# Kernel tuning notes

Measured on AMD Instinct MI355X. Metric: run time of the kernel, lower is better.

Reference implementation:

```python
import jax, jax.numpy as jnp
import numpy as np

B, T, P = 16, 200, 100          # batch, timesteps, MAX_CODE_LEN paths
EMB = 100                        # per-table embedding dim
D = 3 * EMB                      # concatenated path-context dim = 300
NODE_VOCAB = 20000 + 2
PATH_VOCAB = 50000 + 2
SKILL = 30                       # self.skill_n
Q = 50                           # questions (rnn_first_part width)
OUT = 50                         # output_dim


def setup_inputs() -> dict:
    key = jax.random.key(0)
    ks = jax.random.split(key, 14)
    lin = lambda k, fi, fo: jax.random.uniform(k, (fi, fo), jnp.float32, -1.0, 1.0) / np.sqrt(fi)
    vec = lambda k, fi, fo: jax.random.uniform(k, (fo,), jnp.float32, -1.0, 1.0) / np.sqrt(fi)
    return {
        "x_float": jax.random.normal(ks[0], (B, T, Q), jnp.float32),
        "c2v_idx": jax.random.randint(ks[1], (B, T, P, 3), 0, NODE_VOCAB, jnp.int32),
        "embed_nodes": jax.random.normal(ks[2], (NODE_VOCAB, EMB), jnp.float32),
        "embed_paths": jax.random.normal(ks[3], (PATH_VOCAB, EMB), jnp.float32),
        "W_trans": lin(ks[4], D, D), "b_trans": vec(ks[5], D, D),
        "W_att": lin(ks[6], D, 1), "b_att": vec(ks[7], D, 1),
        "W_skill": lin(ks[8], D, SKILL), "b_skill": vec(ks[9], D, SKILL),
        "W_kc": lin(ks[10], Q, SKILL) + 0.15, "b_kc": vec(ks[11], Q, SKILL),
        "W_pred": lin(ks[12], SKILL, OUT), "b_pred": vec(ks[13], SKILL, OUT),
    }


def reference(x_float, c2v_idx, embed_nodes, embed_paths, W_trans, b_trans,
              W_att, b_att, W_skill, b_skill, W_kc, b_kc, W_pred, b_pred):
    # gather three embeddings per path triple  -> [B,T,P,100] each
    start_e = embed_nodes[c2v_idx[..., 0]]
    path_e = embed_paths[c2v_idx[..., 1]]
    end_e = embed_nodes[c2v_idx[..., 2]]
    full_embed = jnp.concatenate([start_e, end_e, path_e], axis=-1)   # [B,T,P,300]

    # path transformation + attention scores
    transformed = jnp.tanh(full_embed @ W_trans + b_trans)            # [B,T,P,300]
    context_w = transformed @ W_att + b_att                           # [B,T,P,1]
    # NOTE: original uses nn.Softmax(dim=1) -> softmax over the TIME axis
    attn = jax.nn.softmax(context_w, axis=1)                          # [B,T,P,1]
    code_vectors = jnp.sum(full_embed * attn, axis=2)                 # [B,T,300]

    kc_mask = jax.nn.sigmoid(x_float @ W_kc + b_kc)                   # [B,T,30]
    out = code_vectors @ W_skill + b_skill                            # [B,T,30]
    res2 = out * (kc_mask >= 0.5).astype(out.dtype)                   # hard-gated skills
    res = jax.nn.sigmoid(res2 @ W_pred + b_pred)                      # [B,T,50]
    return (res, res2, kc_mask, attn)
```

## Files before the change

### kernel.cpp

```cpp
#include <hip/hip_runtime.h>
#include <hip/hip_bf16.h>
#include <math.h>

#define Bdim 16
#define Tdim 200
#define Pdim 100
#define EMB  100
#define Ddim 300
#define SKILL 30
#define Qdim 50
#define OUTD 50

#define OFF_RES   0
#define OFF_RES2  (Bdim*Tdim*OUTD)
#define OFF_KC    (OFF_RES2 + Bdim*Tdim*SKILL)
#define OFF_ATTN  (OFF_KC + Bdim*Tdim*SKILL)

typedef __bf16 bf16x8 __attribute__((ext_vector_type(8)));
typedef __bf16 bf16x4 __attribute__((ext_vector_type(4)));
typedef float  f32x4  __attribute__((ext_vector_type(4)));

#define BM    128
#define KPAD  320
#define ASTR  312
#define TPB   512

#define EROW  320

#define NROWS (Bdim*Tdim*Pdim)
#define WBT_BYTES ((size_t)KPAD*KPAD*2)
#define E_BYTES   ((size_t)NROWS*EROW*2)

__device__ __forceinline__ float fast_tanh(float x) {
    float t = __expf(2.0f * x);
    return 1.0f - 2.0f * __builtin_amdgcn_rcpf(t + 1.0f);
}
__device__ __forceinline__ float sigmoidf_(float z) {
    return 1.f / (1.f + expf(-z));
}

__global__ __launch_bounds__(256) void prep_wbt_kernel(
    const float* __restrict__ Wt, __bf16* __restrict__ wbt)
{
    int id = blockIdx.x * 256 + threadIdx.x;
    if (id >= KPAD * KPAD) return;
    int j = id / KPAD, k = id - j * KPAD;
    float v = (j < Ddim && k < Ddim) ? Wt[k * Ddim + j] : 0.0f;
    wbt[id] = (__bf16)v;
}

template <bool WRITE_E>
__global__ __launch_bounds__(TPB, 4) void score_mfma_kernel(
    const int*    __restrict__ c2v,
    const float*  __restrict__ en,
    const float*  __restrict__ ep,
    const __bf16* __restrict__ wbt,
    const float*  __restrict__ bt,
    const float*  __restrict__ wa,
    const float*  __restrict__ ba,
    float* __restrict__ scores,
    __bf16* __restrict__ e_out)
{
    __shared__ __align__(16) __bf16 A_lds[BM * ASTR];
    __shared__ __align__(16) char   aux_lds[2048];
    int*  idx_lds = (int*)aux_lds;
    float (*red_lds)[BM] = (float (*)[BM])aux_lds;

    const int tid = threadIdx.x;
    const int m0  = blockIdx.x * BM;

    if (tid < BM * 3) idx_lds[tid] = c2v[(size_t)m0 * 3 + tid];
    __syncthreads();

    {
        const int r   = tid >> 2;
        const int sub = tid & 3;
        const int i0 = idx_lds[r * 3 + 0];
        const int i1 = idx_lds[r * 3 + 1];
        const int i2 = idx_lds[r * 3 + 2];
        __bf16* arow = &A_lds[r * ASTR];
        const float* srcs[3] = { en + (size_t)i0 * EMB,
                                 en + (size_t)i2 * EMB,
                                 ep + (size_t)i1 * EMB };
        #pragma unroll
        for (int seg = 0; seg < 3; ++seg) {
            const float* src = srcs[seg];
            float4 v[7];
            #pragma unroll
            for (int k = 0; k < 7; ++k) {
                int j = sub + 4 * k;
                if (j < 25) v[k] = *(const float4*)(src + j * 4);
            }
            #pragma unroll
            for (int k = 0; k < 7; ++k) {
                int j = sub + 4 * k;
                if (j < 25) {
                    float4 w = v[k];
                    bf16x4 b4 = { (__bf16)w.x, (__bf16)w.y, (__bf16)w.z, (__bf16)w.w };
                    *(bf16x4*)(arow + seg * 100 + j * 4) = b4;
                }
            }
        }
        if (sub < 3) *(bf16x4*)(arow + 300 + sub * 4) = (bf16x4){};
    }
    __syncthreads();

    if (WRITE_E) {
        #pragma unroll
        for (int pos = tid; pos < BM * 40; pos += TPB) {
            int r = pos / 40, q = pos - r * 40;
            bf16x8 v = *(const bf16x8*)&A_lds[r * ASTR + q * 8];
            *(bf16x8*)&e_out[(size_t)(m0 + r) * EROW + q * 8] = v;
        }
    }

    const int wid = tid >> 6, lane = tid & 63;
    const int wm = wid >> 2, wn = wid & 3;
    const int lr = lane & 15, lg = lane >> 4;

    f32x4 acc[4][5];
    #pragma unroll
    for (int mf = 0; mf < 4; ++mf)
        #pragma unroll
        for (int nf = 0; nf < 5; ++nf) acc[mf][nf] = (f32x4){0.f, 0.f, 0.f, 0.f};

    #pragma unroll
    for (int kt = 0; kt < 10; ++kt) {
        const int k0 = kt * 32;
        bf16x8 bfr[5];
        #pragma unroll
        for (int nf = 0; nf < 5; ++nf)
            bfr[nf] = *(const bf16x8*)&wbt[(size_t)(wn * 80 + nf * 16 + lr) * KPAD + k0 + lg * 8];
        bf16x8 af[4];
        #pragma unroll
        for (int mf = 0; mf < 4; ++mf) {
            bf16x8 a = *(const bf16x8*)&A_lds[(wm * 64 + mf * 16 + lr) * ASTR + k0 + lg * 8];
            if (kt == 9 && lg == 3) a = (bf16x8){};
            af[mf] = a;
        }
        #pragma unroll
        for (int mf = 0; mf < 4; ++mf)
            #pragma unroll
            for (int nf = 0; nf < 5; ++nf)
                acc[mf][nf] = __builtin_amdgcn_mfma_f32_16x16x32_bf16(
                    af[mf], bfr[nf], acc[mf][nf], 0, 0, 0);
    }

    float btv[5], wav[5];
    #pragma unroll
    for (int nf = 0; nf < 5; ++nf) {
        int c = wn * 80 + nf * 16 + lr;
        bool ok = (c < Ddim);
        btv[nf] = ok ? bt[c] : 0.f;
        wav[nf] = ok ? wa[c] : 0.f;
    }
    float sred[4][4];
    #pragma unroll
    for (int mf = 0; mf < 4; ++mf) {
        #pragma unroll
        for (int i = 0; i < 4; ++i) {
            float s = 0.f;
            #pragma unroll
            for (int nf = 0; nf < 5; ++nf)
                s += fast_tanh(acc[mf][nf][i] + btv[nf]) * wav[nf];
            s += __shfl_xor(s, 1, 64);
            s += __shfl_xor(s, 2, 64);
            s += __shfl_xor(s, 4, 64);
            s += __shfl_xor(s, 8, 64);
            sred[mf][i] = s;
        }
    }
    __syncthreads();
    #pragma unroll
    for (int mf = 0; mf < 4; ++mf)
        #pragma unroll
        for (int i = 0; i < 4; ++i)
            if (lr == 0) red_lds[wn][wm * 64 + mf * 16 + lg * 4 + i] = sred[mf][i];
    __syncthreads();
    for (int r = tid; r < BM; r += TPB) {
        float s = ba[0] + red_lds[0][r] + red_lds[1][r] + red_lds[2][r] + red_lds[3][r];
        scores[m0 + r] = s;
    }
}

__global__ __launch_bounds__(64) void softmax_time_kernel(float* __restrict__ a)
{
    const int b = blockIdx.x / Pdim;
    const int p = blockIdx.x - b * Pdim;
    const int lane = threadIdx.x;
    const size_t base = (size_t)b * Tdim * Pdim + p;

    float v[4];
    float m = -1e30f;
    #pragma unroll
    for (int i = 0; i < 4; ++i) {
        int t = lane + i * 64;
        v[i] = (t < Tdim) ? a[base + (size_t)t * Pdim] : -1e30f;
        m = fmaxf(m, v[i]);
    }
    #pragma unroll
    for (int off = 32; off > 0; off >>= 1) m = fmaxf(m, __shfl_xor(m, off, 64));

    float s = 0.f;
    #pragma unroll
    for (int i = 0; i < 4; ++i) {
        int t = lane + i * 64;
        if (t < Tdim) { v[i] = expf(v[i] - m); s += v[i]; }
    }
    #pragma unroll
    for (int off = 32; off > 0; off >>= 1) s += __shfl_xor(s, off, 64);

    const float inv = 1.f / s;
    #pragma unroll
    for (int i = 0; i < 4; ++i) {
        int t = lane + i * 64;
        if (t < Tdim) a[base + (size_t)t * Pdim] = v[i] * inv;
    }
}

template <bool USE_E>
__global__ __launch_bounds__(512, 4) void cvpred4_kernel(
    const float*  __restrict__ x,
    const int*    __restrict__ c2v,
    const float*  __restrict__ en,
    const float*  __restrict__ ep,
    const __bf16* __restrict__ E,
    const float*  __restrict__ attn,
    const float* __restrict__ Wsk, const float* __restrict__ bsk,
    const float* __restrict__ Wkc, const float* __restrict__ bkc,
    const float* __restrict__ Wpr, const float* __restrict__ bpr,
    float* __restrict__ res, float* __restrict__ res2, float* __restrict__ kcm)
{
    const int bt_i = blockIdx.x;
    const int tid  = threadIdx.x;

    __shared__ float  wsk_lds[Ddim * SKILL];
    __shared__ float  wkc_lds[Qdim * SKILL];
    __shared__ float  wpr_lds[SKILL * OUTD];
    __shared__ int    idx_lds[Pdim * 3];
    __shared__ float  attn_lds[Pdim];
    __shared__ float  x_lds[Qdim];
    __shared__ float4 part_lds[6][76];
    __shared__ float  cv_lds[Ddim];
    __shared__ float  zk_lds[SKILL], o_lds[SKILL], r2_lds[SKILL];

    const int pg = tid / 75;
    const int ch = tid - pg * 75;

    for (int i = tid; i < (Ddim * SKILL) / 4; i += 512)
        ((float4*)wsk_lds)[i] = ((const float4*)Wsk)[i];
    for (int i = tid; i < (Qdim * SKILL) / 4; i += 512)
        ((float4*)wkc_lds)[i] = ((const float4*)Wkc)[i];
    for (int i = tid; i < (SKILL * OUTD) / 4; i += 512)
        ((float4*)wpr_lds)[i] = ((const float4*)Wpr)[i];
    if (!USE_E) {
        if (tid < Pdim * 3) idx_lds[tid] = c2v[(size_t)bt_i * (Pdim * 3) + tid];
    }
    if (tid >= 320 && tid < 320 + Pdim) attn_lds[tid - 320] = attn[(size_t)bt_i * Pdim + tid - 320];
    if (tid >= 448 && tid < 448 + Qdim) x_lds[tid - 448] = x[(size_t)bt_i * Qdim + tid - 448];

    bf16x4 ev[17];
    if (USE_E && pg < 6) {
        const __bf16* base = E + (size_t)bt_i * (Pdim * EROW) + ch * 4;
        #pragma unroll
        for (int k = 0; k < 17; ++k) {
            int p = pg + 6 * k;
            if (p < Pdim) ev[k] = *(const bf16x4*)(base + p * EROW);
        }
    }
    __syncthreads();

    if (pg < 6) {
        float4 acc = {0.f, 0.f, 0.f, 0.f};
        if (USE_E) {
            #pragma unroll
            for (int k = 0; k < 17; ++k) {
                int p = pg + 6 * k;
                if (p < Pdim) {
                    float a = attn_lds[p];
                    acc.x = fmaf(a, (float)ev[k].x, acc.x);
                    acc.y = fmaf(a, (float)ev[k].y, acc.y);
                    acc.z = fmaf(a, (float)ev[k].z, acc.z);
                    acc.w = fmaf(a, (float)ev[k].w, acc.w);
                }
            }
        } else {
            const int seg = ch / 25, cq = ch - seg * 25;
            const float* tab = (seg == 2) ? ep : en;
            const int io = (seg == 0) ? 0 : (seg == 1) ? 2 : 1;
            int   ri[17];
            float rw[17];
            #pragma unroll
            for (int k = 0; k < 17; ++k) {
                int p = pg + 6 * k;
                bool ok = (p < Pdim);
                ri[k] = idx_lds[(ok ? p : 0) * 3 + io];
                rw[k] = ok ? attn_lds[p] : 0.f;
            }
            {
                float4 va[9];
                #pragma unroll
                for (int k = 0; k < 9; ++k)
                    va[k] = *(const float4*)&tab[(size_t)ri[k] * EMB + cq * 4];
                #pragma unroll
                for (int k = 0; k < 9; ++k) {
                    acc.x = fmaf(rw[k], va[k].x, acc.x);
                    acc.y = fmaf(rw[k], va[k].y, acc.y);
                    acc.z = fmaf(rw[k], va[k].z, acc.z);
                    acc.w = fmaf(rw[k], va[k].w, acc.w);
                }
            }
            {
                float4 vb[8];
                #pragma unroll
                for (int k = 0; k < 8; ++k)
                    vb[k] = *(const float4*)&tab[(size_t)ri[k + 9] * EMB + cq * 4];
                #pragma unroll
                for (int k = 0; k < 8; ++k) {
                    acc.x = fmaf(rw[k + 9], vb[k].x, acc.x);
                    acc.y = fmaf(rw[k + 9], vb[k].y, acc.y);
                    acc.z = fmaf(rw[k + 9], vb[k].z, acc.z);
                    acc.w = fmaf(rw[k + 9], vb[k].w, acc.w);
                }
            }
        }
        part_lds[pg][ch] = acc;
    }
    __syncthreads();

    if (tid < 75) {
        float4 a0 = part_lds[0][tid], a1 = part_lds[1][tid];
        float4 a2 = part_lds[2][tid], a3 = part_lds[3][tid];
        float4 a4 = part_lds[4][tid], a5 = part_lds[5][tid];
        int c = tid * 4;
        cv_lds[c + 0] = a0.x + a1.x + a2.x + a3.x + a4.x + a5.x;
        cv_lds[c + 1] = a0.y + a1.y + a2.y + a3.y + a4.y + a5.y;
        cv_lds[c + 2] = a0.z + a1.z + a2.z + a3.z + a4.z + a5.z;
        cv_lds[c + 3] = a0.w + a1.w + a2.w + a3.w + a4.w + a5.w;
    }
    __syncthreads();

    if (tid < 480) {
        const int s = tid >> 4, l = tid & 15;
        float o = 0.f;
        #pragma unroll
        for (int j = 0; j < 19; ++j) {
            int c = l + 16 * j;
            if (c < Ddim) o = fmaf(cv_lds[c], wsk_lds[c * SKILL + s], o);
        }
        o += __shfl_xor(o, 8, 64);
        o += __shfl_xor(o, 4, 64);
        o += __shfl_xor(o, 2, 64);
        o += __shfl_xor(o, 1, 64);
        if (l == 0) o_lds[s] = o + bsk[s];
    }
    if (tid < 240) {
        const int s = tid >> 3, l = tid & 7;
        float zk = 0.f;
        #pragma unroll
        for (int j = 0; j < 7; ++j) {
            int q = l + 8 * j;
            if (q < Qdim) zk = fmaf(x_lds[q], wkc_lds[q * SKILL + s], zk);
        }
        zk += __shfl_xor(zk, 4, 64);
        zk += __shfl_xor(zk, 2, 64);
        zk += __shfl_xor(zk, 1, 64);
        if (l == 0) zk_lds[s] = zk + bkc[s];
    }
    __syncthreads();

    if (tid < SKILL) {
        float zk = zk_lds[tid];
        float r2 = (zk >= 0.f) ? o_lds[tid] : 0.f;
        kcm [(size_t)bt_i * SKILL + tid] = sigmoidf_(zk);
        res2[(size_t)bt_i * SKILL + tid] = r2;
        r2_lds[tid] = r2;
    }
    __syncthreads();

    if (tid < 400) {
        const int od = tid >> 3, l = tid & 7;
        float z = 0.f;
        #pragma unroll
        for (int j = 0; j < 4; ++j) {
            int s = l + 8 * j;
            if (s < SKILL) z = fmaf(r2_lds[s], wpr_lds[s * OUTD + od], z);
        }
        z += __shfl_xor(z, 4, 64);
        z += __shfl_xor(z, 2, 64);
        z += __shfl_xor(z, 1, 64);
        if (l == 0) res[(size_t)bt_i * OUTD + od] = sigmoidf_(z + bpr[od]);
    }
}

extern "C" void kernel_launch(void* const* d_in, const int* in_sizes, int n_in,
                              void* d_out, int out_size, void* d_ws, size_t ws_size,
                              hipStream_t stream)
{
    const float* x   = (const float*)d_in[0];
    const int*   c2v = (const int*)  d_in[1];
    const float* en  = (const float*)d_in[2];
    const float* ep  = (const float*)d_in[3];
    const float* Wt  = (const float*)d_in[4];
    const float* bt  = (const float*)d_in[5];
    const float* Wa  = (const float*)d_in[6];
    const float* ba  = (const float*)d_in[7];
    const float* Wsk = (const float*)d_in[8];
    const float* bsk = (const float*)d_in[9];
    const float* Wkc = (const float*)d_in[10];
    const float* bkc = (const float*)d_in[11];
    const float* Wpr = (const float*)d_in[12];
    const float* bpr = (const float*)d_in[13];

    float* out  = (float*)d_out;
    float* res  = out + OFF_RES;
    float* res2 = out + OFF_RES2;
    float* kcm  = out + OFF_KC;
    float* attn = out + OFF_ATTN;

    __bf16* wbt  = (__bf16*)d_ws;
    __bf16* e_ws = (__bf16*)((char*)d_ws + WBT_BYTES);

    const bool use_e = ws_size >= WBT_BYTES + E_BYTES;

    prep_wbt_kernel<<<(KPAD * KPAD + 255) / 256, 256, 0, stream>>>(Wt, wbt);

    if (use_e)
        score_mfma_kernel<true><<<NROWS / BM, TPB, 0, stream>>>(
            c2v, en, ep, wbt, bt, Wa, ba, attn, e_ws);
    else
        score_mfma_kernel<false><<<NROWS / BM, TPB, 0, stream>>>(
            c2v, en, ep, wbt, bt, Wa, ba, attn, e_ws);

    softmax_time_kernel<<<Bdim * Pdim, 64, 0, stream>>>(attn);

    if (use_e)
        cvpred4_kernel<true><<<Bdim * Tdim, 512, 0, stream>>>(
            x, c2v, en, ep, e_ws, attn, Wsk, bsk, Wkc, bkc, Wpr, bpr, res, res2, kcm);
    else
        cvpred4_kernel<false><<<Bdim * Tdim, 512, 0, stream>>>(
            x, c2v, en, ep, e_ws, attn, Wsk, bsk, Wkc, bkc, Wpr, bpr, res, res2, kcm);
}
```

Before: 328.0 us.

## Precompute per-path skill projections in score GEMM instead of storing embeddings

Uses linearity: the attention-weighted sum of embeddings projected by W_skill equals the attention-weighted sum of per-path projections. W_skill is appended to the bf16 weight matrix, and the score MFMA kernel computes a 32-wide per-path skill projection that it writes to workspace, replacing the 320-wide bf16 embedding dump. A new cvpred5 kernel then only reduces 30 values per path instead of 300, which cuts workspace write and read traffic. The cost is extra MFMAs in two of the four N-wave groups and bf16 rounding applied before the skill projection.

```diff
diff --git a/kernel.cpp b/kernel.cpp
--- a/kernel.cpp
+++ b/kernel.cpp
@@ -22,14 +22,15 @@
 
 #define BM    128
 #define KPAD  320
+#define WROWS 352
 #define ASTR  312
 #define TPB   512
 
-#define EROW  320
+#define ESW   32
 
 #define NROWS (Bdim*Tdim*Pdim)
-#define WBT_BYTES ((size_t)KPAD*KPAD*2)
-#define E_BYTES   ((size_t)NROWS*EROW*2)
+#define WBT_BYTES ((size_t)WROWS*KPAD*2)
+#define ES_BYTES  ((size_t)NROWS*ESW*4)
 
 __device__ __forceinline__ float fast_tanh(float x) {
     float t = __expf(2.0f * x);
@@ -40,16 +41,23 @@
 }
 
 __global__ __launch_bounds__(256) void prep_wbt_kernel(
-    const float* __restrict__ Wt, __bf16* __restrict__ wbt)
+    const float* __restrict__ Wt, const float* __restrict__ Wsk,
+    __bf16* __restrict__ wbt)
 {
     int id = blockIdx.x * 256 + threadIdx.x;
-    if (id >= KPAD * KPAD) return;
+    if (id >= WROWS * KPAD) return;
     int j = id / KPAD, k = id - j * KPAD;
-    float v = (j < Ddim && k < Ddim) ? Wt[k * Ddim + j] : 0.0f;
+    float v = 0.0f;
+    if (j < KPAD) {
+        if (j < Ddim && k < Ddim) v = Wt[k * Ddim + j];
+    } else {
+        int s = j - KPAD;
+        if (s < SKILL && k < Ddim) v = Wsk[k * SKILL + s];
+    }
     wbt[id] = (__bf16)v;
 }
 
-template <bool WRITE_E>
+template <bool WRITE_ES>
 __global__ __launch_bounds__(TPB, 4) void score_mfma_kernel(
     const int*    __restrict__ c2v,
     const float*  __restrict__ en,
@@ -59,7 +67,7 @@
     const float*  __restrict__ wa,
     const float*  __restrict__ ba,
     float* __restrict__ scores,
-    __bf16* __restrict__ e_out)
+    float* __restrict__ es_out)
 {
     __shared__ __align__(16) __bf16 A_lds[BM * ASTR];
     __shared__ __align__(16) char   aux_lds[2048];
@@ -105,24 +113,19 @@
     }
     __syncthreads();
 
-    if (WRITE_E) {
-        #pragma unroll
-        for (int pos = tid; pos < BM * 40; pos += TPB) {
-            int r = pos / 40, q = pos - r * 40;
-            bf16x8 v = *(const bf16x8*)&A_lds[r * ASTR + q * 8];
-            *(bf16x8*)&e_out[(size_t)(m0 + r) * EROW + q * 8] = v;
-        }
-    }
-
     const int wid = tid >> 6, lane = tid & 63;
     const int wm = wid >> 2, wn = wid & 3;
     const int lr = lane & 15, lg = lane >> 4;
+    const bool do_es = WRITE_ES && (wn < 2);
 
     f32x4 acc[4][5];
-    #pragma unroll
-    for (int mf = 0; mf < 4; ++mf)
+    f32x4 acc_es[4];
+    #pragma unroll
+    for (int mf = 0; mf < 4; ++mf) {
         #pragma unroll
         for (int nf = 0; nf < 5; ++nf) acc[mf][nf] = (f32x4){0.f, 0.f, 0.f, 0.f};
+        acc_es[mf] = (f32x4){0.f, 0.f, 0.f, 0.f};
+    }
 
     #pragma unroll
     for (int kt = 0; kt < 10; ++kt) {
@@ -144,6 +147,24 @@
             for (int nf = 0; nf < 5; ++nf)
                 acc[mf][nf] = __builtin_amdgcn_mfma_f32_16x16x32_bf16(
                     af[mf], bfr[nf], acc[mf][nf], 0, 0, 0);
+        if (do_es) {
+            bf16x8 bes = *(const bf16x8*)&wbt[(size_t)(KPAD + wn * 16 + lr) * KPAD + k0 + lg * 8];
+            #pragma unroll
+            for (int mf = 0; mf < 4; ++mf)
+                acc_es[mf] = __builtin_amdgcn_mfma_f32_16x16x32_bf16(
+                    af[mf], bes, acc_es[mf], 0, 0, 0);
+        }
+    }
+
+    if (do_es) {
+        #pragma unroll
+        for (int mf = 0; mf < 4; ++mf)
+            #pragma unroll
+            for (int i = 0; i < 4; ++i) {
+                int row = wm * 64 + mf * 16 + lg * 4 + i;
+                int col = wn * 16 + lr;
+                es_out[(size_t)(m0 + row) * ESW + col] = acc_es[mf][i];
+            }
     }
 
     float btv[5], wav[5];
@@ -218,13 +239,97 @@
     }
 }
 
-template <bool USE_E>
+__global__ __launch_bounds__(512, 4) void cvpred5_kernel(
+    const float* __restrict__ x,
+    const float* __restrict__ ES,
+    const float* __restrict__ attn,
+    const float* __restrict__ bsk,
+    const float* __restrict__ Wkc, const float* __restrict__ bkc,
+    const float* __restrict__ Wpr, const float* __restrict__ bpr,
+    float* __restrict__ res, float* __restrict__ res2, float* __restrict__ kcm)
+{
+    const int bt_i = blockIdx.x;
+    const int tid  = threadIdx.x;
+
+    __shared__ float es_lds[Pdim * 33];
+    __shared__ float wkc_lds[Qdim * SKILL];
+    __shared__ float wpr_lds[SKILL * OUTD];
+    __shared__ float attn_lds[Pdim];
+    __shared__ float x_lds[Qdim];
+    __shared__ float zk_lds[SKILL], o_lds[SKILL], r2_lds[SKILL];
+
+    {
+        const float* src = ES + (size_t)bt_i * (Pdim * ESW);
+        #pragma unroll
+        for (int pos = tid; pos < Pdim * ESW; pos += 512)
+            es_lds[(pos >> 5) * 33 + (pos & 31)] = src[pos];
+    }
+    for (int i = tid; i < (Qdim * SKILL) / 4; i += 512)
+        ((float4*)wkc_lds)[i] = ((const float4*)Wkc)[i];
+    for (int i = tid; i < (SKILL * OUTD) / 4; i += 512)
+        ((float4*)wpr_lds)[i] = ((const float4*)Wpr)[i];
+    if (tid < Pdim) attn_lds[tid] = attn[(size_t)bt_i * Pdim + tid];
+    if (tid >= 128 && tid < 128 + Qdim) x_lds[tid - 128] = x[(size_t)bt_i * Qdim + tid - 128];
+    __syncthreads();
+
+    if (tid < 480) {
+        const int s = tid >> 4, l = tid & 15;
+        float o = 0.f;
+        #pragma unroll
+        for (int k = 0; k < 7; ++k) {
+            int p = l + 16 * k;
+            if (p < Pdim) o = fmaf(attn_lds[p], es_lds[p * 33 + s], o);
+        }
+        o += __shfl_xor(o, 8, 64);
+        o += __shfl_xor(o, 4, 64);
+        o += __shfl_xor(o, 2, 64);
+        o += __shfl_xor(o, 1, 64);
+        if (l == 0) o_lds[s] = o + bsk[s];
+    }
+    if (tid < 240) {
+        const int s = tid >> 3, l = tid & 7;
+        float zk = 0.f;
+        #pragma unroll
+        for (int j = 0; j < 7; ++j) {
+            int q = l + 8 * j;
+            if (q < Qdim) zk = fmaf(x_lds[q], wkc_lds[q * SKILL + s], zk);
+        }
+        zk += __shfl_xor(zk, 4, 64);
+        zk += __shfl_xor(zk, 2, 64);
+        zk += __shfl_xor(zk, 1, 64);
+        if (l == 0) zk_lds[s] = zk + bkc[s];
+    }
+    __syncthreads();
+
+    if (tid < SKILL) {
+        float zk = zk_lds[tid];
+        float r2 = (zk >= 0.f) ? o_lds[tid] : 0.f;
+        kcm [(size_t)bt_i * SKILL + tid] = sigmoidf_(zk);
+        res2[(size_t)bt_i * SKILL + tid] = r2;
+        r2_lds[tid] = r2;
+    }
+    __syncthreads();
+
+    if (tid < 400) {
+        const int od = tid >> 3, l = tid & 7;
+        float z = 0.f;
+        #pragma unroll
+        for (int j = 0; j < 4; ++j) {
+            int s = l + 8 * j;
+            if (s < SKILL) z = fmaf(r2_lds[s], wpr_lds[s * OUTD + od], z);
+        }
+        z += __shfl_xor(z, 4, 64);
+        z += __shfl_xor(z, 2, 64);
+        z += __shfl_xor(z, 1, 64);
+        if (l == 0) res[(size_t)bt_i * OUTD + od] = sigmoidf_(z + bpr[od]);
+    }
+}
+
 __global__ __launch_bounds__(512, 4) void cvpred4_kernel(
     const float*  __restrict__ x,
     const int*    __restrict__ c2v,
     const float*  __restrict__ en,
     const float*  __restrict__ ep,
-    const __bf16* __restrict__ E,
     const float*  __restrict__ attn,
     const float* __restrict__ Wsk, const float* __restrict__ bsk,
     const float* __restrict__ Wkc, const float* __restrict__ bkc,
@@ -253,75 +358,49 @@
         ((float4*)wkc_lds)[i] = ((const float4*)Wkc)[i];
     for (int i = tid; i < (SKILL * OUTD) / 4; i += 512)
         ((float4*)wpr_lds)[i] = ((const float4*)Wpr)[i];
-    if (!USE_E) {
-        if (tid < Pdim * 3) idx_lds[tid] = c2v[(size_t)bt_i * (Pdim * 3) + tid];
-    }
+    if (tid < Pdim * 3) idx_lds[tid] = c2v[(size_t)bt_i * (Pdim * 3) + tid];
     if (tid >= 320 && tid < 320 + Pdim) attn_lds[tid - 320] = attn[(size_t)bt_i * Pdim + tid - 320];
     if (tid >= 448 && tid < 448 + Qdim) x_lds[tid - 448] = x[(size_t)bt_i * Qdim + tid - 448];
-
-    bf16x4 ev[17];
-    if (USE_E && pg < 6) {
-        const __bf16* base = E + (size_t)bt_i * (Pdim * EROW) + ch * 4;
+    __syncthreads();
+
+    if (pg < 6) {
+        const int seg = ch / 25, cq = ch - seg * 25;
+        const float* tab = (seg == 2) ? ep : en;
+        const int io = (seg == 0) ? 0 : (seg == 1) ? 2 : 1;
+        int   ri[17];
+        float rw[17];
         #pragma unroll
         for (int k = 0; k < 17; ++k) {
             int p = pg + 6 * k;
-            if (p < Pdim) ev[k] = *(const bf16x4*)(base + p * EROW);
-        }
-    }
-    __syncthreads();
-
-    if (pg < 6) {
+            bool ok = (p < Pdim);
+            ri[k] = idx_lds[(ok ? p : 0) * 3 + io];
+            rw[k] = ok ? attn_lds[p] : 0.f;
+        }
         float4 acc = {0.f, 0.f, 0.f, 0.f};
-        if (USE_E) {
-            #pragma unroll
-            for (int k = 0; k < 17; ++k) {
-                int p = pg + 6 * k;
-                if (p < Pdim) {
-                    float a = attn_lds[p];
-                    acc.x = fmaf(a, (float)ev[k].x, acc.x);
-                    acc.y = fmaf(a, (float)ev[k].y, acc.y);
-                    acc.z = fmaf(a, (float)ev[k].z, acc.z);
-                    acc.w = fmaf(a, (float)ev[k].w, acc.w);
-                }
+        {
+            float4 va[9];
+            #pragma unroll
+            for (int k = 0; k < 9; ++k)
+                va[k] = *(const float4*)&tab[(size_t)ri[k] * EMB + cq * 4];
+            #pragma unroll
+            for (int k = 0; k < 9; ++k) {
+                acc.x = fmaf(rw[k], va[k].x, acc.x);
+                acc.y = fmaf(rw[k], va[k].y, acc.y);
+                acc.z = fmaf(rw[k], va[k].z, acc.z);
+                acc.w = fmaf(rw[k], va[k].w, acc.w);
             }
-        } else {
-            const int seg = ch / 25, cq = ch - seg * 25;
-            const float* tab = (seg == 2) ? ep : en;
-            const int io = (seg == 0) ? 0 : (seg == 1) ? 2 : 1;
-            int   ri[17];
-            float rw[17];
-            #pragma unroll
-            for (int k = 0; k < 17; ++k) {
-                int p = pg + 6 * k;
-                bool ok = (p < Pdim);
-                ri[k] = idx_lds[(ok ? p : 0) * 3 + io];
-                rw[k] = ok ? attn_lds[p] : 0.f;
-            }
-            {
-                float4 va[9];
-                #pragma unroll
-                for (int k = 0; k < 9; ++k)
-                    va[k] = *(const float4*)&tab[(size_t)ri[k] * EMB + cq * 4];
-                #pragma unroll
-                for (int k = 0; k < 9; ++k) {
-                    acc.x = fmaf(rw[k], va[k].x, acc.x);
-                    acc.y = fmaf(rw[k], va[k].y, acc.y);
-                    acc.z = fmaf(rw[k], va[k].z, acc.z);
-                    acc.w = fmaf(rw[k], va[k].w, acc.w);
-                }
-            }
-            {
-                float4 vb[8];
-                #pragma unroll
-                for (int k = 0; k < 8; ++k)
-                    vb[k] = *(const float4*)&tab[(size_t)ri[k + 9] * EMB + cq * 4];
-                #pragma unroll
-                for (int k = 0; k < 8; ++k) {
-                    acc.x = fmaf(rw[k + 9], vb[k].x, acc.x);
-                    acc.y = fmaf(rw[k + 9], vb[k].y, acc.y);
-                    acc.z = fmaf(rw[k + 9], vb[k].z, acc.z);
-                    acc.w = fmaf(rw[k + 9], vb[k].w, acc.w);
-                }
+        }
+        {
+            float4 vb[8];
+            #pragma unroll
+            for (int k = 0; k < 8; ++k)
+                vb[k] = *(const float4*)&tab[(size_t)ri[k + 9] * EMB + cq * 4];
+            #pragma unroll
+            for (int k = 0; k < 8; ++k) {
+                acc.x = fmaf(rw[k + 9], vb[k].x, acc.x);
+                acc.y = fmaf(rw[k + 9], vb[k].y, acc.y);
+                acc.z = fmaf(rw[k + 9], vb[k].z, acc.z);
+                acc.w = fmaf(rw[k + 9], vb[k].w, acc.w);
             }
         }
         part_lds[pg][ch] = acc;
@@ -418,26 +497,26 @@
     float* kcm  = out + OFF_KC;
     float* attn = out + OFF_ATTN;
 
-    __bf16* wbt  = (__bf16*)d_ws;
-    __bf16* e_ws = (__bf16*)((char*)d_ws + WBT_BYTES);
-
-    const bool use_e = ws_size >= WBT_BYTES + E_BYTES;
-
-    prep_wbt_kernel<<<(KPAD * KPAD + 255) / 256, 256, 0, stream>>>(Wt, wbt);
-
-    if (use_e)
+    __bf16* wbt   = (__bf16*)d_ws;
+    float*  es_ws = (float*)((char*)d_ws + WBT_BYTES);
+
+    const bool use_es = ws_size >= WBT_BYTES + ES_BYTES;
+
+    prep_wbt_kernel<<<(WROWS * KPAD + 255) / 256, 256, 0, stream>>>(Wt, Wsk, wbt);
+
+    if (use_es)
         score_mfma_kernel<true><<<NROWS / BM, TPB, 0, stream>>>(
-            c2v, en, ep, wbt, bt, Wa, ba, attn, e_ws);
+            c2v, en, ep, wbt, bt, Wa, ba, attn, es_ws);
     else
         score_mfma_kernel<false><<<NROWS / BM, TPB, 0, stream>>>(
-            c2v, en, ep, wbt, bt, Wa, ba, attn, e_ws);
+            c2v, en, ep, wbt, bt, Wa, ba, attn, es_ws);
 
     softmax_time_kernel<<<Bdim * Pdim, 64, 0, stream>>>(attn);
 
-    if (use_e)
-        cvpred4_kernel<true><<<Bdim * Tdim, 512, 0, stream>>>(
-            x, c2v, en, ep, e_ws, attn, Wsk, bsk, Wkc, bkc, Wpr, bpr, res, res2, kcm);
+    if (use_es)
+        cvpred5_kernel<<<Bdim * Tdim, 512, 0, stream>>>(
+            x, es_ws, attn, bsk, Wkc, bkc, Wpr, bpr, res, res2, kcm);
     else
-        cvpred4_kernel<false><<<Bdim * Tdim, 512, 0, stream>>>(
-            x, c2v, en, ep, e_ws, attn, Wsk, bsk, Wkc, bkc, Wpr, bpr, res, res2, kcm);
-}
+        cvpred4_kernel<<<Bdim * Tdim, 512, 0, stream>>>(
+            x, c2v, en, ep, attn, Wsk, bsk, Wkc, bkc, Wpr, bpr, res, res2, kcm);
+}
```

Result: slower. 420.3 us (+28.2%).
